# Optimization experiments

Measured on AMD Instinct MI355X. Metric: run time of the kernel, lower is better.

## Reference

```python
import jax, jax.numpy as jnp
import numpy as np

EMBED = 512
HEADS = 8
DIM_HEAD = 64          # embed_dim // 8
LANDMARKS = 256        # embed_dim // 2
PINV_ITERS = 6
RES_K = 33             # nystrom residual_conv_kernel default
SCALE = DIM_HEAD ** -0.5


def layer_norm(x, g, b, eps=1e-5):
    mu = x.mean(-1, keepdims=True)
    var = ((x - mu) ** 2).mean(-1, keepdims=True)
    return (x - mu) / jnp.sqrt(var + eps) * g + b


def moore_penrose_pinv(x, iters=PINV_ITERS):
    # iterative Moore-Penrose pseudo-inverse (lucidrains nystrom-attention)
    ax = jnp.abs(x)
    z = jnp.swapaxes(x, -1, -2) / (ax.sum(-1).max() * ax.sum(-2).max())
    I = jnp.eye(x.shape[-1], dtype=x.dtype)
    for _ in range(iters):
        xz = x @ z
        z = 0.25 * z @ (13. * I - xz @ (15. * I - xz @ (7. * I - xz)))
    return z


def nystrom_attention(x, w_qkv, w_out, b_out, res_k):
    b, n, _ = x.shape
    m = LANDMARKS
    pad = (m - n % m) % m
    xp = jnp.pad(x, ((0, 0), (pad, 0), (0, 0)))  # left-pad like F.pad(..., padding, 0)
    np_ = n + pad
    qkv = (xp @ w_qkv).reshape(b, np_, 3, HEADS, DIM_HEAD)
    q = qkv[:, :, 0].transpose(0, 2, 1, 3) * SCALE   # [b,h,np,dh]
    k = qkv[:, :, 1].transpose(0, 2, 1, 3)
    v = qkv[:, :, 2].transpose(0, 2, 1, 3)
    l = np_ // m
    q_l = q.reshape(b, HEADS, m, l, DIM_HEAD).mean(3)  # [b,h,m,dh]
    k_l = k.reshape(b, HEADS, m, l, DIM_HEAD).mean(3)
    attn1 = jax.nn.softmax(jnp.einsum('bhid,bhjd->bhij', q, k_l), -1)    # [b,h,np,m]
    attn2 = jax.nn.softmax(jnp.einsum('bhid,bhjd->bhij', q_l, k_l), -1)  # [b,h,m,m]
    attn3 = jax.nn.softmax(jnp.einsum('bhid,bhjd->bhij', q_l, k), -1)    # [b,h,m,np]
    out = (attn1 @ moore_penrose_pinv(attn2)) @ (attn3 @ v)              # [b,h,np,dh]
    # depthwise residual conv over the sequence dim, per head (shared across dh)
    v_c = v.transpose(0, 3, 1, 2).reshape(b * DIM_HEAD, HEADS, np_)
    res = jax.lax.conv_general_dilated(
        v_c, res_k[:, None, :], (1,), [(RES_K // 2, RES_K // 2)],
        dimension_numbers=('NCH', 'OIH', 'NCH'), feature_group_count=HEADS)
    out = out + res.reshape(b, DIM_HEAD, HEADS, np_).transpose(0, 2, 3, 1)
    out = out.transpose(0, 2, 1, 3).reshape(b, np_, HEADS * DIM_HEAD)
    out = out @ w_out + b_out
    return out[:, -n:]  # drop left padding


def dwconv2d(x, w, b, k):
    # x: [B,C,H,W], w: [C,1,k,k] depthwise
    y = jax.lax.conv_general_dilated(
        x, w, (1, 1), [(k // 2, k // 2)] * 2,
        dimension_numbers=('NCHW', 'OIHW', 'NCHW'), feature_group_count=x.shape[1])
    return y + b[None, :, None, None]


def ppeg(x, H, W, w7, b7, w5, b5, w3, b3):
    B, _, C = x.shape
    cls_tok, feat = x[:, :1], x[:, 1:]
    f = feat.transpose(0, 2, 1).reshape(B, C, H, W)
    y = f + dwconv2d(f, w7, b7, 7) + dwconv2d(f, w5, b5, 5) + dwconv2d(f, w3, b3, 3)
    y = y.reshape(B, C, H * W).transpose(0, 2, 1)
    return jnp.concatenate([cls_tok, y], axis=1)


def reference(h, w_fc1, b_fc1, cls_token,
              ln1_g, ln1_b, qkv1_w, out1_w, out1_b, res1_k,
              conv7_w, conv7_b, conv5_w, conv5_b, conv3_w, conv3_b,
              ln2_g, ln2_b, qkv2_w, out2_w, out2_b, res2_k,
              lnf_g, lnf_b):
    h = jax.nn.relu(h @ w_fc1 + b_fc1)                 # [B,N,512]
    B, N, C = h.shape
    _H = int(np.ceil(np.sqrt(N)))
    add = _H * _H - N
    h = jnp.concatenate([h, h[:, :add]], axis=1)       # square padding
    h = jnp.concatenate([jnp.broadcast_to(cls_token, (B, 1, C)), h], axis=1)
    h = h + nystrom_attention(layer_norm(h, ln1_g, ln1_b), qkv1_w, out1_w, out1_b, res1_k)
    h = ppeg(h, _H, _H, conv7_w, conv7_b, conv5_w, conv5_b, conv3_w, conv3_b)
    h = h + nystrom_attention(layer_norm(h, ln2_g, ln2_b), qkv2_w, out2_w, out2_b, res2_k)
    return layer_norm(h, lnf_g, lnf_b)[:, 0]           # [B,512]


def setup_inputs() -> dict:
    key = jax.random.key(0)
    ks = jax.random.split(key, 24)
    B, N, IN_DIM = 2, 4096, 1024
    w = lambda k, shape, s=0.02: jax.random.normal(k, shape, jnp.float32) * s
    z = lambda shape: jnp.zeros(shape, jnp.float32)
    o = lambda shape: jnp.ones(shape, jnp.float32)
    return {
        'h': jax.random.normal(ks[0], (B, N, IN_DIM), jnp.float32),
        'w_fc1': w(ks[1], (IN_DIM, EMBED)), 'b_fc1': z((EMBED,)),
        'cls_token': w(ks[2], (1, 1, EMBED)),
        'ln1_g': o((EMBED,)), 'ln1_b': z((EMBED,)),
        'qkv1_w': w(ks[3], (EMBED, 3 * HEADS * DIM_HEAD)),
        'out1_w': w(ks[4], (HEADS * DIM_HEAD, EMBED)), 'out1_b': z((EMBED,)),
        'res1_k': w(ks[5], (HEADS, RES_K), 0.1),
        'conv7_w': w(ks[6], (EMBED, 1, 7, 7), 0.05), 'conv7_b': z((EMBED,)),
        'conv5_w': w(ks[7], (EMBED, 1, 5, 5), 0.05), 'conv5_b': z((EMBED,)),
        'conv3_w': w(ks[8], (EMBED, 1, 3, 3), 0.05), 'conv3_b': z((EMBED,)),
        'ln2_g': o((EMBED,)), 'ln2_b': z((EMBED,)),
        'qkv2_w': w(ks[9], (EMBED, 3 * HEADS * DIM_HEAD)),
        'out2_w': w(ks[10], (HEADS * DIM_HEAD, EMBED)), 'out2_b': z((EMBED,)),
        'res2_k': w(ks[11], (HEADS, RES_K), 0.1),
        'lnf_g': o((EMBED,)), 'lnf_b': z((EMBED,)),
    }
```

## Files before the change

kernel.cpp:

```cpp
#include <hip/hip_runtime.h>
#include <hip/hip_bf16.h>

#define HEADS 8
#define DH 64
#define EMB 512
#define NP 4352
#define NTOK 4097
#define PADF 255
#define LM 256
#define SCALE 0.125f

typedef __attribute__((ext_vector_type(8))) short bf8;
typedef __attribute__((ext_vector_type(4))) float f4;
typedef __attribute__((ext_vector_type(8))) unsigned short us8;
typedef __attribute__((ext_vector_type(4))) unsigned short us4;
typedef unsigned short u16;

__device__ __forceinline__ u16 f2b(float f){
  union { float f; unsigned u; } x; x.f = f;
  unsigned r = x.u + 0x7fffu + ((x.u>>16)&1u);
  return (u16)(r>>16);
}
__device__ __forceinline__ float b2f(u16 h){
  union { unsigned u; float f; } x; x.u = ((unsigned)h)<<16;
  return x.f;
}

__device__ __forceinline__ void gload_lds(const u16* g, u16* l){
  __builtin_amdgcn_global_load_lds((const __attribute__((address_space(1))) void*)g,
                                   (__attribute__((address_space(3))) void*)l, 16, 0, 0);
}

#define WAITCNT(N) asm volatile("s_waitcnt vmcnt(" #N ")" ::: "memory")
#define SCHED_FENCE() __builtin_amdgcn_sched_barrier(0)
#define BARRIER() __builtin_amdgcn_s_barrier()

template<int MODE>
__global__ __launch_bounds__(256)
void k_g128(const u16* __restrict__ A, const u16* __restrict__ B,
            float* __restrict__ C, u16* __restrict__ C16,
            int K, int lda, int ldb, int ldc,
            long sAb, long sAh, long sBb, long sBh, long sCb, long sCh, int nh,
            float alpha, const float* __restrict__ bias, int relu, int rowoff,
            int nx, int ksplit)
{
  int z = blockIdx.z;
  const u16* Ab = A + (long)(z/nh)*sAb + (long)(z%nh)*sAh;
  const u16* Bb = B + (long)(z/nh)*sBb + (long)(z%nh)*sBh;
  long cb = (long)(z/nh)*sCb + (long)(z%nh)*sCh;
  int bx = blockIdx.x % nx, kc = blockIdx.x / nx;
  int m0 = blockIdx.y*128, n0 = bx*128;
  int klen = K/ksplit, kbeg = kc*klen, nch = klen/32;
  __shared__ u16 As[3][4096];
  __shared__ u16 Bs[3][4096];
  int tid=threadIdx.x, w=tid>>6, lane=tid&63, q=lane>>4, lr=lane&15;
  int wrow=(w>>1)*64, wcol=(w&1)*64;
  int srow = tid>>2, scol = (tid&3)*8;
  const u16* ga  = Ab + (long)(m0+srow)*lda + kbeg + scol;
  const u16* ga2 = Ab + (long)(m0+64+srow)*lda + kbeg + scol;
  const u16* gb  = Bb + (long)(n0+srow)*ldb + kbeg + scol;
  const u16* gb2 = Bb + (long)(n0+64+srow)*ldb + kbeg + scol;
  int lo = srow*32 + scol;
  f4 acc[4][4] = {};
  auto stage = [&](int r, int c){
    gload_lds(ga  + c*32, &As[r][lo]);
    gload_lds(ga2 + c*32, &As[r][2048+lo]);
    gload_lds(gb  + c*32, &Bs[r][lo]);
    gload_lds(gb2 + c*32, &Bs[r][2048+lo]);
// ... 86 lines not shown
      acc[t] = __builtin_amdgcn_mfma_f32_16x16x32_bf16(af, bfr, acc[t], 0,0,0);
    }
  };
  stage(0,0);
  if(nch>1) stage(1,1);
  if(nch>2) stage(2,2);
  int bufc = 0;
  for(int c=0;c<nch;c++){
    int rem = nch-1-c;
    if(rem>=2) WAITCNT(4); else if(rem==1) WAITCNT(2); else WAITCNT(0);
    SCHED_FENCE();
    BARRIER();
    compute(bufc);
    SCHED_FENCE();
    BARRIER();
    SCHED_FENCE();
    if(c+3<nch) stage(bufc, c+3);
    bufc = (bufc+1==3)?0:bufc+1;
  }
  #pragma unroll
  for(int t=0;t<4;t++){
    #pragma unroll
    for(int e=0;e<4;e++){
      int gm = m0 + w*16 + q*4 + e;
      int gn = n0 + t*16 + lr;
      float v = acc[t][e]*alpha;
      if(MODE==0) C[cb + (long)gm*ldc + gn] = v;
      else if(MODE==2) C16[cb + (long)gm*ldc + gn] = f2b(v);
      else if(MODE==3) atomicAdd(&C[cb + (long)gm*ldc + gn], v);
      else if(MODE==5){
        v += bias[gn];
        if(gm>=rowoff) C[cb + (long)(gm-rowoff)*ldc + gn] += v;
      }
    }
  }
}

__global__ __launch_bounds__(256)
void k_pg3(const u16* __restrict__ Ah, const u16* __restrict__ Al,
           const u16* __restrict__ Bh, const u16* __restrict__ Bl,
           u16* __restrict__ Oh, u16* __restrict__ Ol, float na, float nd,
           u16* __restrict__ TOh, u16* __restrict__ TOl, float ta, float td)
{
  long zo = (long)blockIdx.z*65536;
  int m0 = blockIdx.y*32, n0 = blockIdx.x*64;
  __shared__ u16 S[3][6144];
  int tid=threadIdx.x, w=tid>>6, lane=tid&63, q=lane>>4, lr=lane&15;
  int t2 = tid & 127;
  const u16* srcA = (tid<128 ? Ah : Al) + zo + (long)(m0 + (t2>>2))*256 + (t2&3)*8;
  const u16* srcBh = Bh + zo + (long)(n0 + (tid>>2))*256 + (tid&3)*8;
  const u16* srcBl = Bl + zo + (long)(n0 + (tid>>2))*256 + (tid&3)*8;
  f4 acc[2] = {};
  auto stage = [&](int r, int c){
    gload_lds(srcA  + c*32, &S[r][tid*8]);
    gload_lds(srcBh + c*32, &S[r][2048 + tid*8]);
    gload_lds(srcBl + c*32, &S[r][4096 + tid*8]);
  };
  int mrow = (w>>1)*16 + lr;
  auto compute = [&](int r){
    bf8 ah = *(const bf8*)&S[r][mrow*32 + q*8];
    bf8 al = *(const bf8*)&S[r][1024 + mrow*32 + q*8];
    #pragma unroll
    for(int t=0;t<2;t++){
      int nrow = (w&1)*32 + t*16 + lr;
      bf8 bh = *(const bf8*)&S[r][2048 + nrow*32 + q*8];
      bf8 bl = *(const bf8*)&S[r][4096 + nrow*32 + q*8];
      acc[t] = __builtin_amdgcn_mfma_f32_16x16x32_bf16(ah, bh, acc[t], 0,0,0);
      acc[t] = __builtin_amdgcn_mfma_f32_16x16x32_bf16(ah, bl, acc[t], 0,0,0);
      acc[t] = __builtin_amdgcn_mfma_f32_16x16x32_bf16(al, bh, acc[t], 0,0,0);
    }
  };
  stage(0,0);
  stage(1,1);
  stage(2,2);
  int bufc = 0;
  for(int c=0;c<8;c++){
    int rem = 7-c;
    if(rem>=2) WAITCNT(6); else if(rem==1) WAITCNT(3); else WAITCNT(0);
    SCHED_FENCE();
    BARRIER();
// ... 2 lines not shown
    BARRIER();
    SCHED_FENCE();
    if(c+3<8) stage(bufc, c+3);
    bufc = (bufc+1==3)?0:bufc+1;
  }
  #pragma unroll
  for(int t=0;t<2;t++){
    int gn = n0 + (w&1)*32 + t*16 + lr;
    if(Oh){
      #pragma unroll
      for(int r=0;r<4;r++){
        int gm = m0 + (w>>1)*16 + q*4 + r;
        float v = na*acc[t][r] + ((gm==gn)?nd:0.f);
        u16 h = f2b(v);
        long o = zo + (long)gm*256 + gn;
        Oh[o] = h; Ol[o] = f2b(v - b2f(h));
      }
    }
    if(TOh){
      us4 th, tl;
      #pragma unroll
      for(int r=0;r<4;r++){
        int gm = m0 + (w>>1)*16 + q*4 + r;
        float v = ta*acc[t][r] + ((gm==gn)?td:0.f);
        u16 h = f2b(v);
        th[r] = h; tl[r] = f2b(v - b2f(h));
      }
      long o = zo + (long)gn*256 + (m0 + (w>>1)*16 + q*4);
      *(us4*)&TOh[o] = th; *(us4*)&TOl[o] = tl;
    }
  }
}

__global__ __launch_bounds__(256)
void k_pg3b(const u16* __restrict__ Zh, const u16* __restrict__ Zl,
            const u16* __restrict__ Ph, const u16* __restrict__ Pl,
            const u16* __restrict__ Bh, const u16* __restrict__ Bl,
            u16* __restrict__ Ozh, u16* __restrict__ Ozl,
            u16* __restrict__ Oyh, u16* __restrict__ Oyl,
            u16* __restrict__ Tyh, u16* __restrict__ Tyl)
{
  long zo = (long)blockIdx.z*65536;
  int ysel = blockIdx.y>>3;
  int m0 = (blockIdx.y&7)*32, n0 = blockIdx.x*64;
  const u16* Ah = ysel ? Ph : Zh;
  const u16* Al = ysel ? Pl : Zl;
  __shared__ u16 S[3][6144];
  int tid=threadIdx.x, w=tid>>6, lane=tid&63, q=lane>>4, lr=lane&15;
  int t2 = tid & 127;
  const u16* srcA = (tid<128 ? Ah : Al) + zo + (long)(m0 + (t2>>2))*256 + (t2&3)*8;
  const u16* srcBh = Bh + zo + (long)(n0 + (tid>>2))*256 + (tid&3)*8;
  const u16* srcBl = Bl + zo + (long)(n0 + (tid>>2))*256 + (tid&3)*8;
  f4 acc[2] = {};
  auto stage = [&](int r, int c){
    gload_lds(srcA  + c*32, &S[r][tid*8]);
    gload_lds(srcBh + c*32, &S[r][2048 + tid*8]);
    gload_lds(srcBl + c*32, &S[r][4096 + tid*8]);
  };
  int mrow = (w>>1)*16 + lr;
  auto compute = [&](int r){
    bf8 ah = *(const bf8*)&S[r][mrow*32 + q*8];
    bf8 al = *(const bf8*)&S[r][1024 + mrow*32 + q*8];
    #pragma unroll
    for(int t=0;t<2;t++){
      int nrow = (w&1)*32 + t*16 + lr;
      bf8 bh = *(const bf8*)&S[r][2048 + nrow*32 + q*8];
      bf8 bl = *(const bf8*)&S[r][4096 + nrow*32 + q*8];
      acc[t] = __builtin_amdgcn_mfma_f32_16x16x32_bf16(ah, bh, acc[t], 0,0,0);
      acc[t] = __builtin_amdgcn_mfma_f32_16x16x32_bf16(ah, bl, acc[t], 0,0,0);
      acc[t] = __builtin_amdgcn_mfma_f32_16x16x32_bf16(al, bh, acc[t], 0,0,0);
    }
  };
  stage(0,0);
  stage(1,1);
  stage(2,2);
  int bufc = 0;
  for(int c=0;c<8;c++){
    int rem = 7-c;
    if(rem>=2) WAITCNT(6); else if(rem==1) WAITCNT(3); else WAITCNT(0);
    SCHED_FENCE();
    BARRIER();
    compute(bufc);
    SCHED_FENCE();
    BARRIER();
    SCHED_FENCE();
    if(c+3<8) stage(bufc, c+3);
    bufc = (bufc+1==3)?0:bufc+1;
  }
  #pragma unroll
  for(int t=0;t<2;t++){
    int gn = n0 + (w&1)*32 + t*16 + lr;
    if(!ysel){
      #pragma unroll
      for(int r=0;r<4;r++){
        int gm = m0 + (w>>1)*16 + q*4 + r;
        float v = 0.25f*acc[t][r];
        u16 h = f2b(v);
        long o = zo + (long)gm*256 + gn;
        Ozh[o] = h; Ozl[o] = f2b(v - b2f(h));
      }
    } else {
      us4 th, tl;
      #pragma unroll
      for(int r=0;r<4;r++){
        int gm = m0 + (w>>1)*16 + q*4 + r;
        float v = 0.25f*acc[t][r];
        u16 h = f2b(v);
        long o = zo + (long)gm*256 + gn;
        Oyh[o] = h; Oyl[o] = f2b(v - b2f(h));
        float tv = -v + ((gm==gn)?7.f:0.f);
        u16 h2 = f2b(tv);
        th[r] = h2; tl[r] = f2b(tv - b2f(h2));
      }
      long o = zo + (long)gn*256 + (m0 + (w>>1)*16 + q*4);
      *(us4*)&Tyh[o] = th; *(us4*)&Tyl[o] = tl;
    }
  }
}

__global__ __launch_bounds__(256)
void k_att2f(const u16* __restrict__ ql, const u16* __restrict__ kl,
             float* __restrict__ att2, float* __restrict__ colsum)
{
  int z = blockIdx.y;
  int m0 = blockIdx.x*64;
  __shared__ u16 SQ[64*64];
  __shared__ u16 SKL[256*64];
  int tid=threadIdx.x, w=tid>>6, lane=tid&63, q=lane>>4, lr=lane&15;
  {
    const u16* qb = ql + (long)z*16384 + m0*64;
    #pragma unroll
    for(int p=0;p<2;p++){
      int idx = tid + p*256; int row = idx>>3; int js = ((idx&7)^(row&7))<<3;
      gload_lds(qb + row*64 + js, &SQ[idx*8]);
    }
    const u16* kb = kl + (long)z*16384;
    #pragma unroll
    for(int p=0;p<8;p++){
      int idx = tid + p*256; int row = idx>>3; int js = ((idx&7)^(row&7))<<3;
      gload_lds(kb + row*64 + js, &SKL[idx*8]);
    }
  }
  __syncthreads();
  f4 acc[16] = {};
  {
    int ar = w*16+lr;
    bf8 af0 = *(const bf8*)&SQ[ar*64 + ((q^(ar&7))<<3)];
    bf8 af1 = *(const bf8*)&SQ[ar*64 + (((q|4)^(ar&7))<<3)];
    #pragma unroll
// ... 165 lines not shown
    #pragma unroll
    for(int kc=0;kc<17;kc++){ mm[kc]=pm[(z*17+kc)*256 + j]; M=fmaxf(M,mm[kc]); }
    float s = 0.f;
    #pragma unroll
    for(int kc=0;kc<17;kc++){ float e=expf(mm[kc]-M); wk[tid][kc]=e; s+=e*pl[(z*17+kc)*256 + j]; }
    float inv = 1.f/s;
    #pragma unroll
    for(int kc=0;kc<17;kc++) wk[tid][kc]*=inv;
  }
  __syncthreads();
  float acc[8];
  #pragma unroll
  for(int p=0;p<8;p++) acc[p]=0.f;
  for(int kc=0;kc<17;kc++){
    long base = ((long)(z*17+kc)*256 + j0)*64;
    #pragma unroll
    for(int p=0;p<8;p++){
      int idx = tid + p*128;
      acc[p] += wk[idx>>6][kc]*partO[base + idx];
    }
  }
  #pragma unroll
  for(int p=0;p<8;p++){ int idx = tid + p*128; T[idx>>6][idx&63] = f2b(acc[p]); }
  __syncthreads();
  int d = tid>>1, jh = (tid&1)*8;
  us8 vv;
  #pragma unroll
  for(int u=0;u<8;u++) vv[u] = T[jh+u][d];
  *(us8*)&avbT16[(long)(z*64+d)*256 + j0 + jh] = vv;
}

__global__ __launch_bounds__(256)
void k_att1(const u16* __restrict__ qkv16, const u16* __restrict__ kl,
            const u16* __restrict__ zavT, float* __restrict__ Qc)
{
  int z = blockIdx.y, b = z>>3, h = z&7;
  int m0 = blockIdx.x*64;
  __shared__ u16 SQ[64*64];
  __shared__ u16 SKL[256*64];
  __shared__ u16 SZV[64*256];
  int tid=threadIdx.x, w=tid>>6, lane=tid&63, q=lane>>4, lr=lane&15;
  {
    const u16* qb = qkv16 + (long)b*NP*1536 + h*64;
    #pragma unroll
    for(int p=0;p<2;p++){
      int idx = tid + p*256; int row = idx>>3; int js = ((idx&7)^(row&7))<<3;
      gload_lds(qb + (long)(m0+row)*1536 + js, &SQ[idx*8]);
    }
    const u16* kb = kl + (long)z*16384;
    #pragma unroll
    for(int p=0;p<8;p++){
      int idx = tid + p*256; int row = idx>>3; int js = ((idx&7)^(row&7))<<3;
      gload_lds(kb + row*64 + js, &SKL[idx*8]);
    }
    const u16* zb = zavT + (long)z*16384;
    #pragma unroll
    for(int p=0;p<8;p++){
      int idx = tid + p*256; int row = idx>>5; int cs = ((idx&31)^(row&7))<<3;
      gload_lds(zb + row*256 + cs, &SZV[idx*8]);
    }
  }
  __syncthreads();
  f4 acc[16] = {};
  {
    int ar = w*16+lr;
    bf8 af0 = *(const bf8*)&SQ[ar*64 + ((q^(ar&7))<<3)];
    bf8 af1 = *(const bf8*)&SQ[ar*64 + (((q|4)^(ar&7))<<3)];
// ... 19 lines not shown
  #pragma unroll
  for(int t=0;t<16;t++)
    #pragma unroll
    for(int e=0;e<4;e++){ float p = expf(acc[t][e]*SCALE - mx[e]); acc[t][e]=p; sm[e]+=p; }
  #pragma unroll
  for(int s=1;s<16;s<<=1)
    #pragma unroll
    for(int e=0;e<4;e++) sm[e] += __shfl_xor(sm[e], s);
  float inv[4];
  #pragma unroll
  for(int e=0;e<4;e++) inv[e] = 1.f/sm[e];
  __syncthreads();
  u16* PS = SKL;
  #pragma unroll
  for(int t=0;t<16;t++)
    #pragma unroll
    for(int e=0;e<4;e++){
      int prow = w*16 + q*4 + e, pcol = t*16 + lr;
      PS[prow*256 + (((pcol>>3)^(prow&7))<<3) + (pcol&7)] = f2b(acc[t][e]*inv[e]);
    }
  __syncthreads();
  f4 acc2[4] = {};
  int pr = w*16+lr;
  #pragma unroll
  for(int ks=0;ks<8;ks++){
    bf8 af = *(const bf8*)&PS[pr*256 + (((ks*4+q)^(pr&7))<<3)];
    #pragma unroll
    for(int t=0;t<4;t++){
      int rr = t*16+lr;
      bf8 bf_ = *(const bf8*)&SZV[rr*256 + (((ks*4+q)^(rr&7))<<3)];
      acc2[t] = __builtin_amdgcn_mfma_f32_16x16x32_bf16(af, bf_, acc2[t], 0,0,0);
    }
  }
  #pragma unroll
  for(int t=0;t<4;t++)
    #pragma unroll
    for(int r=0;r<4;r++){
      int gm = m0 + w*16 + q*4 + r;
      int gd = t*16 + lr;
      Qc[((long)b*NP + gm)*512 + h*64 + gd] = acc2[t][r];
    }
}

__global__ void k_wT(const float* __restrict__ in, u16* __restrict__ out, int K, int N){
  int n0=blockIdx.x*32, k0=blockIdx.y*32, tid=threadIdx.x;
  __shared__ float T[32][33];
  int lr=tid&31, lc=tid>>5;
  #pragma unroll
  for(int p=0;p<4;p++) T[lc+8*p][lr] = in[(long)(k0+lc+8*p)*N + n0+lr];
  __syncthreads();
  #pragma unroll
  for(int p=0;p<4;p++) out[(long)(n0+lc+8*p)*K + k0+lr] = f2b(T[lr][lc+8*p]);
}

__global__ __launch_bounds__(256)
void k_vT(const u16* __restrict__ qkv16, u16* __restrict__ vT){
  int t0=blockIdx.x*64, h=blockIdx.y, b=blockIdx.z, tid=threadIdx.x;
  __shared__ u16 T[64][72];
  const u16* src = qkv16 + (long)b*NP*1536 + 1024 + h*64;
  for(int s=0;s<2;s++){
    int idx=tid+s*256; int row=idx>>3, c8=(idx&7)*8;
    *(us8*)&T[row][c8] = *(const us8*)&src[(long)(t0+row)*1536 + c8];
  }
  __syncthreads();
  u16* dst = vT + ((long)(b*8+h)*64)*NP;
  int d = tid>>2, j0=(tid&3)*16;
  us8 v0,v1;
  #pragma unroll
  for(int jj=0;jj<8;jj++){ v0[jj]=T[j0+jj][d]; v1[jj]=T[j0+8+jj][d]; }
  *(us8*)&dst[(long)d*NP + t0 + j0]     = v0;
  *(us8*)&dst[(long)d*NP + t0 + j0 + 8] = v1;
}

__global__ void k_cvt16(const float* __restrict__ in, u16* __restrict__ out, long n){
  long i = (long)blockIdx.x*256 + threadIdx.x;
  if(i<n) out[i] = f2b(in[i]);
}

__global__ void k_cls(const float* __restrict__ cls, float* __restrict__ seq){
  int b = blockIdx.x;
  seq[(long)b*NTOK*EMB + threadIdx.x] = cls[threadIdx.x];
}

__global__ void k_ln_pad(const float* __restrict__ seq, u16* __restrict__ xp,
                         const float* __restrict__ g, const float* __restrict__ bb){
  int b = blockIdx.y, i = blockIdx.x, tid = threadIdx.x;
  u16* out = xp + ((long)b*NP + i)*EMB;
  if(i < PADF){ out[tid]=0; out[tid+256]=0; return; }
  const float* x = seq + ((long)b*NTOK + (i-PADF))*EMB;
  float v0 = x[tid], v1 = x[tid+256];
  __shared__ float red[256];
  red[tid]=v0+v1; __syncthreads();
  for(int s=128;s>0;s>>=1){ if(tid<s) red[tid]+=red[tid+s]; __syncthreads(); }
  float mu = red[0]*(1.0f/512.0f); __syncthreads();
  float d0=v0-mu, d1=v1-mu;
  red[tid]=d0*d0+d1*d1; __syncthreads();
  for(int s=128;s>0;s>>=1){ if(tid<s) red[tid]+=red[tid+s]; __syncthreads(); }
  float rstd = rsqrtf(red[0]*(1.0f/512.0f) + 1e-5f);
  out[tid]     = f2b(d0*rstd*g[tid]     + bb[tid]);
  out[tid+256] = f2b(d1*rstd*g[tid+256] + bb[tid+256]);
}

__global__ void k_landmarks(const u16* __restrict__ qkv, u16* __restrict__ q_l, u16* __restrict__ k_l,
                            float* __restrict__ colsum){
  if(blockIdx.y==0 && blockIdx.z==0 && blockIdx.x<16) colsum[blockIdx.x*256 + threadIdx.x] = 0.f;
  int j = blockIdx.x*4 + (threadIdx.x>>6), h = blockIdx.y, b = blockIdx.z, d = threadIdx.x&63;
  const u16* base = qkv + (long)b*NP*1536 + h*64 + d;
  float sq=0.f, sk=0.f;
  for(int l=0;l<17;l++){
    long row = (long)(j*17+l)*1536;
    sq += b2f(base[row]);
    sk += b2f(base[row+512]);
  }
  long o = (((long)b*HEADS + h)*LM + j)*DH + d;
  q_l[o] = f2b(sq * (SCALE/17.0f));
  k_l[o] = f2b(sk * (1.0f/17.0f));
}

__global__ void k_pair_init(const float* __restrict__ att2,
    const float* __restrict__ colsum,
    u16* __restrict__ Xh, u16* __restrict__ Xl,
    u16* __restrict__ Zh, u16* __restrict__ Zl,
    u16* __restrict__ Zth, u16* __restrict__ Ztl)
{
  long zo = (long)blockIdx.z*65536;
  int i0 = blockIdx.y*64, j0 = blockIdx.x*64;
  int tid = threadIdx.x;
  __shared__ float cred[256];
  {
    float cm = 0.f;
    #pragma unroll
    for(int i=0;i<16;i++) cm = fmaxf(cm, colsum[tid + i*256]);
    cred[tid] = cm; __syncthreads();
    for(int s=128;s>0;s>>=1){ if(tid<s) cred[tid]=fmaxf(cred[tid],cred[tid+s]); __syncthreads(); }
  }
  float inv = 1.0f/cred[0];
  __syncthreads();
  __shared__ float T[64][68];
  int li = tid>>2, jc = (tid&3)*16;
  #pragma unroll
  for(int u=0;u<4;u++){
    float4 v = *(const float4*)&att2[zo + (long)(i0+li)*256 + j0 + jc + u*4];
    T[li][jc+u*4]=v.x; T[li][jc+u*4+1]=v.y; T[li][jc+u*4+2]=v.z; T[li][jc+u*4+3]=v.w;
    long o = zo + (long)(i0+li)*256 + j0 + jc + u*4;
    float vv[4] = {v.x,v.y,v.z,v.w};
    us4 xh, xl, zth, ztl;
    #pragma unroll
    for(int c=0;c<4;c++){
      u16 h = f2b(vv[c]); xh[c]=h; xl[c]=f2b(vv[c]-b2f(h));
      float zt = vv[c]*inv;
      u16 h2 = f2b(zt); zth[c]=h2; ztl[c]=f2b(zt-b2f(h2));
    }
    *(us4*)&Xh[o]=xh; *(us4*)&Xl[o]=xl; *(us4*)&Zth[o]=zth; *(us4*)&Ztl[o]=ztl;
  }
  __syncthreads();
  int lj = tid>>2, ic = (tid&3)*16;
  #pragma unroll
  for(int r=0;r<16;r++){
    float x = T[ic+r][lj]*inv;
    u16 h = f2b(x);
    long o = zo + (long)(j0+lj)*256 + i0 + ic + r;
    Zh[o]=h; Zl[o]=f2b(x-b2f(h));
  }
}

__global__ __launch_bounds__(256)
void k_rconv(const u16* __restrict__ qkv16, const float* __restrict__ resk,
             const float* __restrict__ Qin, u16* __restrict__ Qo16){
  int t0 = blockIdx.x*64, h = blockIdx.y, b = blockIdx.z;
  __shared__ float V[96*64];
  const u16* vb = qkv16 + (long)b*NP*1536 + 1024 + h*64;
  int tid = threadIdx.x;
  #pragma unroll
  for(int s=0;s<3;s++){
    int idx = tid + s*256;
    int row = idx>>3, c8 = (idx&7)*8;
    int p = t0 - 16 + row;
    if(p>=0 && p<NP){
      us8 v = *(const us8*)&vb[(long)p*1536 + c8];
      #pragma unroll
      for(int jj=0;jj<8;jj++) V[row*64+c8+jj] = b2f(v[jj]);
    } else {
      #pragma unroll
      for(int jj=0;jj<8;jj++) V[row*64+c8+jj] = 0.f;
    }
  }
  __syncthreads();
  int d = tid&63, lt = (tid>>6)*16;
  float acc[16] = {};
  #pragma unroll
  for(int s=0;s<48;s++){
    float val = V[(lt+s)*64 + d];
    #pragma unroll
    for(int j=0;j<16;j++){
      int tap = s - j;
      if(tap>=0 && tap<33) acc[j] += resk[h*33+tap]*val;
    }
  }
  #pragma unroll
  for(int j=0;j<16;j++){
    long idx = ((long)b*NP + t0 + lt + j)*EMB + h*64 + d;
    Qo16[idx] = f2b(Qin[idx] + acc[j]);
  }
}

__global__ __launch_bounds__(256)
void k_ppeg(const float* __restrict__ seq, float* __restrict__ out,
    const float* __restrict__ w7,const float* __restrict__ b7,
    const float* __restrict__ w5,const float* __restrict__ b5,
    const float* __restrict__ w3,const float* __restrict__ b3){
  int b = blockIdx.z, cg = blockIdx.y;
  int rp = blockIdx.x>>1, xs = blockIdx.x&1;
  int ch0 = cg*64;
  __shared__ float s7[64*49], s5[64*25], s3[64*9], sbias[64];
  int tid = threadIdx.x;
  for(int i=tid;i<64*49;i+=256) s7[i] = w7[ch0*49+i];
  for(int i=tid;i<64*25;i+=256) s5[i] = w5[ch0*25+i];
  for(int i=tid;i<64*9;i+=256)  s3[i] = w3[ch0*9+i];
  if(tid<64) sbias[tid] = b7[ch0+tid]+b5[ch0+tid]+b3[ch0+tid];
  if(cg==0 && blockIdx.x==0){
    out[(long)b*NTOK*EMB + tid]       = seq[(long)b*NTOK*EMB + tid];
    out[(long)b*NTOK*EMB + 256 + tid] = seq[(long)b*NTOK*EMB + 256 + tid];
  }
  __syncthreads();
  int c = tid & 63;
  int y = rp*4 + (tid>>6);
  const float* sbase = seq + (long)b*NTOK*EMB + EMB + (ch0 + c);
  float* obase = out + (long)b*NTOK*EMB + EMB + (ch0 + c);
  const float* W7 = &s7[c*49];
  const float* W5 = &s5[c*25];
  const float* W3 = &s3[c*9];
  float bsum = sbias[c];
  for(int xc=0;xc<4;xc++){
    int xb = xs*32 + xc*8;
    float acc[8];
// ... 21 lines not shown
    #pragma unroll
    for(int j=0;j<8;j++) obase[(long)(y*64+xb+j)*EMB] = acc[j];
  }
}

__global__ void k_final_ln(const float* __restrict__ seq, const float* __restrict__ g,
                           const float* __restrict__ bb, float* __restrict__ out){
  int b = blockIdx.x, tid = threadIdx.x;
  const float* x = seq + (long)b*NTOK*EMB;
  float v0 = x[tid], v1 = x[tid+256];
  __shared__ float red[256];
  red[tid]=v0+v1; __syncthreads();
  for(int s=128;s>0;s>>=1){ if(tid<s) red[tid]+=red[tid+s]; __syncthreads(); }
  float mu = red[0]*(1.0f/512.0f); __syncthreads();
  float d0=v0-mu, d1=v1-mu;
  red[tid]=d0*d0+d1*d1; __syncthreads();
  for(int s=128;s>0;s>>=1){ if(tid<s) red[tid]+=red[tid+s]; __syncthreads(); }
  float rstd = rsqrtf(red[0]*(1.0f/512.0f) + 1e-5f);
  out[b*512+tid]     = d0*rstd*g[tid]     + bb[tid];
  out[b*512+tid+256] = d1*rstd*g[tid+256] + bb[tid+256];
}

extern "C" void kernel_launch(void* const* d_in, const int* in_sizes, int n_in,
                              void* d_out, int out_size, void* d_ws, size_t ws_size,
                              hipStream_t stream) {
  const float* in[24];
  for(int i=0;i<24;i++) in[i] = (const float*)d_in[i];

  float* W = (float*)d_ws;
  size_t off = 0;
  float* seqA = W+off; off += 4195328;
  float* seqB = W+off; off += 4195328;
  float* att2 = W+off; off += 1048576;
  float* Qc   = W+off; off += 4456448;
  float* partO= W+off; off += 17825792;
  float* pm   = W+off; off += 69632;
  float* pl   = W+off; off += 69632;
  u16* xpb    = (u16*)(W+off); off += 2228224;
  u16* qkvb16 = (u16*)(W+off); off += 6684672;
  u16* vT16   = (u16*)(W+off); off += 2228224;
  u16* q_l16  = (u16*)(W+off); off += 131072;
  u16* k_l16  = (u16*)(W+off); off += 131072;
  u16* avbT16 = (u16*)(W+off); off += 131072;
  u16* zavT16 = (u16*)(W+off); off += 131072;
  u16* Qc16   = (u16*)(W+off); off += 2228224;
  u16* qkvwT1 = (u16*)(W+off); off += 393216;
  u16* qkvwT2 = (u16*)(W+off); off += 393216;
  u16* outwT1 = (u16*)(W+off); off += 131072;
  u16* outwT2 = (u16*)(W+off); off += 131072;
  u16* pairs  = (u16*)(W+off); off += 9437184;
  float* colsum = W+off; off += 4096;
  if (ws_size < off*sizeof(float)) return;

  u16* h16   = pairs;
  u16* wfc1T = pairs + 8388608;

  const long PB = 1048576;
  u16 *Xh=pairs,        *Xl=pairs+PB;
  u16 *Z0h=pairs+2*PB,  *Z0l=pairs+3*PB;
  u16 *Z0th=pairs+4*PB, *Z0tl=pairs+5*PB;
  u16 *Z1h=pairs+6*PB,  *Z1l=pairs+7*PB;
  u16 *P0h=pairs+8*PB,  *P0l=pairs+9*PB;
  u16 *P1h=pairs+10*PB, *P1l=pairs+11*PB;
  u16 *Tth=pairs+12*PB, *Ttl=pairs+13*PB;
  u16 *Uth=pairs+14*PB, *Utl=pairs+15*PB;
  u16 *Vth=pairs+16*PB, *Vtl=pairs+17*PB;

  k_cvt16<<<32768,256,0,stream>>>(in[0], h16, 8388608L);
  k_wT<<<dim3(16,32),256,0,stream>>>(in[1],  wfc1T, 1024, 512);
  k_wT<<<dim3(48,16),256,0,stream>>>(in[6],  qkvwT1, 512, 1536);
  k_wT<<<dim3(48,16),256,0,stream>>>(in[18], qkvwT2, 512, 1536);
  k_wT<<<dim3(16,16),256,0,stream>>>(in[7],  outwT1, 512, 512);
  k_wT<<<dim3(16,16),256,0,stream>>>(in[19], outwT2, 512, 512);

  k_g128<0><<<dim3(4,32,2),256,0,stream>>>(h16, wfc1T, seqA+EMB, nullptr,
      1024, 1024,1024,512, 4194304L,0, 0,0, (long)NTOK*EMB,0, 1, 1.0f, in[2], 1, 0, 4, 1);
  k_cls<<<2,512,0,stream>>>(in[3], seqA);

  auto attention = [&](float* seq, const float* lng,const float* lnb,
                       const u16* qkvwT, const u16* outwT, const float* outb, const float* resk){
    k_ln_pad<<<dim3(NP,2),256,0,stream>>>(seq, xpb, lng, lnb);
    k_g128<2><<<dim3(12,34,2),256,0,stream>>>(xpb, qkvwT, nullptr, qkvb16,
        512, 512,512,1536, (long)NP*512,0, 0,0, (long)NP*1536,0, 1, 1.0f, nullptr, 0, 0, 12, 1);
    k_landmarks<<<dim3(64,HEADS,2),256,0,stream>>>(qkvb16, q_l16, k_l16, colsum);
    k_vT<<<dim3(68,8,2),256,0,stream>>>(qkvb16, vT16);
    k_att2f<<<dim3(4,16),256,0,stream>>>(q_l16, k_l16, att2, colsum);
    k_pair_init<<<dim3(4,4,16),256,0,stream>>>(att2, colsum, Xh,Xl, Z0h,Z0l, Z0th,Z0tl);
    dim3 pgrid(4,8,16);
    k_pg3<<<pgrid,256,0,stream>>>(Xh,Xl, Z0th,Z0tl, P0h,P0l,1.0f,0.f, Tth,Ttl,-1.0f,7.f);
    for(int it=0; it<6; it++){
      u16 *Zh_=(it&1)?Z1h:Z0h, *Zl_=(it&1)?Z1l:Z0l;
      u16 *Nh_=(it&1)?Z0h:Z1h, *Nl_=(it&1)?Z0l:Z1l;
      u16 *Pch=(it&1)?P1h:P0h, *Pcl=(it&1)?P1l:P0l;
      u16 *Pnh=(it&1)?P0h:P1h, *Pnl=(it&1)?P0l:P1l;
      k_pg3<<<pgrid,256,0,stream>>>(Pch,Pcl, Tth,Ttl, nullptr,nullptr,0.f,0.f, Uth,Utl,-1.0f,15.f);
      k_pg3<<<pgrid,256,0,stream>>>(Pch,Pcl, Uth,Utl, nullptr,nullptr,0.f,0.f, Vth,Vtl,-1.0f,13.f);
      if(it<5) k_pg3b<<<dim3(4,16,16),256,0,stream>>>(Zh_,Zl_, Pch,Pcl, Vth,Vtl,
                                                      Nh_,Nl_, Pnh,Pnl, Tth,Ttl);
      else     k_pg3<<<pgrid,256,0,stream>>>(Zh_,Zl_, Vth,Vtl, Nh_,Nl_,0.25f,0.f,
                                             nullptr,nullptr,0.f,0.f);
    }
    k_att3<<<dim3(17,4,16),256,0,stream>>>(qkvb16, q_l16, vT16, partO, pm, pl);
    k_mrg3<<<dim3(16,16),128,0,stream>>>(partO, pm, pl, avbT16);
    k_g64<2><<<dim3(4,1,16),256,0,stream>>>(avbT16, Z0h, nullptr, zavT16,
        256, 256,256,256, 0,16384L, 0,65536L, 0,16384L, 16, 1.0f, nullptr, 0, 0, 4, 1);
    k_att1<<<dim3(68,16),256,0,stream>>>(qkvb16, k_l16, zavT16, Qc);
    k_rconv<<<dim3(68,8,2),256,0,stream>>>(qkvb16, resk, Qc, Qc16);
    k_g64<5><<<dim3(8,65,2),256,0,stream>>>(Qc16, outwT, seq, nullptr,
        512, 512,512,512, (long)NP*512,0, 0,0, (long)NTOK*EMB,0, 1, 1.0f, outb, PADF, 192, 8, 1);
  };

  attention(seqA, in[4], in[5], qkvwT1, outwT1, in[8], in[9]);
  k_ppeg<<<dim3(32,8,2),256,0,stream>>>(seqA, seqB, in[10],in[11],in[12],in[13],in[14],in[15]);
  attention(seqB, in[16], in[17], qkvwT2, outwT2, in[20], in[21]);
  k_final_ln<<<2,256,0,stream>>>(seqB, in[22], in[23], (float*)d_out);
}
```

Before: 850.1 us.

## Fuse pinv iteration kernels into one persistent kernel with grid barriers

Replaces the roughly 19 separate k_pg3/k_pg3b launches of the Moore-Penrose iteration with a single persistent kernel of 512 blocks that syncs between GEMM stages using a software atomic grid barrier. The barrier counter is reset inside k_landmarks. The goal is to remove per-launch overhead and the tail idle between the many small dependent GEMMs. The change relies on all 512 blocks being co-resident, with launch bounds requesting 2 blocks per CU, or the kernel deadlocks. The Z and P updates now run as two sequential tiles in the same block rather than as a 2x-wide grid.

```diff
diff --git a/kernel.cpp b/kernel.cpp
--- a/kernel.cpp
+++ b/kernel.cpp
@@ -34,6 +34,22 @@
 #define WAITCNT(N) asm volatile("s_waitcnt vmcnt(" #N ")" ::: "memory")
 #define SCHED_FENCE() __builtin_amdgcn_sched_barrier(0)
 #define BARRIER() __builtin_amdgcn_s_barrier()
+
+__device__ __forceinline__ void gridbar(unsigned* bar, unsigned nblk){
+  __syncthreads();
+  if(threadIdx.x==0){
+    __threadfence();
+    unsigned g = atomicAdd(&bar[1], 0u);
+    if(atomicAdd(&bar[0], 1u) == nblk-1u){
+      atomicExch(&bar[0], 0u);
+      atomicAdd(&bar[1], 1u);
+    } else {
+      while(atomicAdd(&bar[1], 0u) == g) __builtin_amdgcn_s_sleep(1);
+    }
+    __threadfence();
+  }
+  __syncthreads();
+}
 
 template<int MODE>
 __global__ __launch_bounds__(256)
@@ -190,16 +206,13 @@
   }
 }
 
-__global__ __launch_bounds__(256)
-void k_pg3(const u16* __restrict__ Ah, const u16* __restrict__ Al,
-           const u16* __restrict__ Bh, const u16* __restrict__ Bl,
-           u16* __restrict__ Oh, u16* __restrict__ Ol, float na, float nd,
-           u16* __restrict__ TOh, u16* __restrict__ TOl, float ta, float td)
+__device__ __forceinline__ void pg3_tile(int tid, int m0, int n0, long zo,
+    const u16* Ah, const u16* Al, const u16* Bh, const u16* Bl,
+    u16* Oh, u16* Ol, float na, float nd,
+    u16* TOh, u16* TOl, float ta, float td,
+    u16 S[3][6144])
 {
-  long zo = (long)blockIdx.z*65536;
-  int m0 = blockIdx.y*32, n0 = blockIdx.x*64;
-  __shared__ u16 S[3][6144];
-  int tid=threadIdx.x, w=tid>>6, lane=tid&63, q=lane>>4, lr=lane&15;
+  int w=tid>>6, lane=tid&63, q=lane>>4, lr=lane&15;
   int t2 = tid & 127;
   const u16* srcA = (tid<128 ? Ah : Al) + zo + (long)(m0 + (t2>>2))*256 + (t2&3)*8;
   const u16* srcBh = Bh + zo + (long)(n0 + (tid>>2))*256 + (tid&3)*8;
@@ -268,89 +281,35 @@
   }
 }
 
-__global__ __launch_bounds__(256)
-void k_pg3b(const u16* __restrict__ Zh, const u16* __restrict__ Zl,
-            const u16* __restrict__ Ph, const u16* __restrict__ Pl,
-            const u16* __restrict__ Bh, const u16* __restrict__ Bl,
-            u16* __restrict__ Ozh, u16* __restrict__ Ozl,
-            u16* __restrict__ Oyh, u16* __restrict__ Oyl,
-            u16* __restrict__ Tyh, u16* __restrict__ Tyl)
+__global__ __launch_bounds__(256, 2)
+void k_pinv_all(const u16* __restrict__ Xh, const u16* __restrict__ Xl,
+                u16* Z0h, u16* Z0l, const u16* __restrict__ Z0th, const u16* __restrict__ Z0tl,
+                u16* Z1h, u16* Z1l,
+                u16* P0h, u16* P0l, u16* P1h, u16* P1l,
+                u16* Tth, u16* Ttl, u16* Uth, u16* Utl, u16* Vth, u16* Vtl,
+                unsigned* bar)
 {
+  __shared__ u16 S[3][6144];
+  int tid = threadIdx.x;
   long zo = (long)blockIdx.z*65536;
-  int ysel = blockIdx.y>>3;
-  int m0 = (blockIdx.y&7)*32, n0 = blockIdx.x*64;
-  const u16* Ah = ysel ? Ph : Zh;
-  const u16* Al = ysel ? Pl : Zl;
-  __shared__ u16 S[3][6144];
-  int tid=threadIdx.x, w=tid>>6, lane=tid&63, q=lane>>4, lr=lane&15;
-  int t2 = tid & 127;
-  const u16* srcA = (tid<128 ? Ah : Al) + zo + (long)(m0 + (t2>>2))*256 + (t2&3)*8;
-  const u16* srcBh = Bh + zo + (long)(n0 + (tid>>2))*256 + (tid&3)*8;
-  const u16* srcBl = Bl + zo + (long)(n0 + (tid>>2))*256 + (tid&3)*8;
-  f4 acc[2] = {};
-  auto stage = [&](int r, int c){
-    gload_lds(srcA  + c*32, &S[r][tid*8]);
-    gload_lds(srcBh + c*32, &S[r][2048 + tid*8]);
-    gload_lds(srcBl + c*32, &S[r][4096 + tid*8]);
-  };
-  int mrow = (w>>1)*16 + lr;
-  auto compute = [&](int r){
-    bf8 ah = *(const bf8*)&S[r][mrow*32 + q*8];
-    bf8 al = *(const bf8*)&S[r][1024 + mrow*32 + q*8];
-    #pragma unroll
-    for(int t=0;t<2;t++){
-      int nrow = (w&1)*32 + t*16 + lr;
-      bf8 bh = *(const bf8*)&S[r][2048 + nrow*32 + q*8];
-      bf8 bl = *(const bf8*)&S[r][4096 + nrow*32 + q*8];
-      acc[t] = __builtin_amdgcn_mfma_f32_16x16x32_bf16(ah, bh, acc[t], 0,0,0);
-      acc[t] = __builtin_amdgcn_mfma_f32_16x16x32_bf16(ah, bl, acc[t], 0,0,0);
-      acc[t] = __builtin_amdgcn_mfma_f32_16x16x32_bf16(al, bh, acc[t], 0,0,0);
-    }
-  };
-  stage(0,0);
-  stage(1,1);
-  stage(2,2);
-  int bufc = 0;
-  for(int c=0;c<8;c++){
-    int rem = 7-c;
-    if(rem>=2) WAITCNT(6); else if(rem==1) WAITCNT(3); else WAITCNT(0);
-    SCHED_FENCE();
-    BARRIER();
-    compute(bufc);
-    SCHED_FENCE();
-    BARRIER();
-    SCHED_FENCE();
-    if(c+3<8) stage(bufc, c+3);
-    bufc = (bufc+1==3)?0:bufc+1;
-  }
-  #pragma unroll
-  for(int t=0;t<2;t++){
-    int gn = n0 + (w&1)*32 + t*16 + lr;
-    if(!ysel){
-      #pragma unroll
-      for(int r=0;r<4;r++){
-        int gm = m0 + (w>>1)*16 + q*4 + r;
-        float v = 0.25f*acc[t][r];
-        u16 h = f2b(v);
-        long o = zo + (long)gm*256 + gn;
-        Ozh[o] = h; Ozl[o] = f2b(v - b2f(h));
-      }
-    } else {
-      us4 th, tl;
-      #pragma unroll
-      for(int r=0;r<4;r++){
-        int gm = m0 + (w>>1)*16 + q*4 + r;
-        float v = 0.25f*acc[t][r];
-        u16 h = f2b(v);
-        long o = zo + (long)gm*256 + gn;
-        Oyh[o] = h; Oyl[o] = f2b(v - b2f(h));
-        float tv = -v + ((gm==gn)?7.f:0.f);
-        u16 h2 = f2b(tv);
-        th[r] = h2; tl[r] = f2b(tv - b2f(h2));
-      }
-      long o = zo + (long)gn*256 + (m0 + (w>>1)*16 + q*4);
-      *(us4*)&Tyh[o] = th; *(us4*)&Tyl[o] = tl;
-    }
+  int m0 = blockIdx.y*32, n0 = blockIdx.x*64;
+  pg3_tile(tid,m0,n0,zo, Xh,Xl, Z0th,Z0tl, P0h,P0l,1.0f,0.f, Tth,Ttl,-1.0f,7.f, S);
+  gridbar(bar, 512);
+  u16 *Zch=Z0h,*Zcl=Z0l,*Znh=Z1h,*Znl=Z1l;
+  u16 *Pch=P0h,*Pcl=P0l,*Pnh=P1h,*Pnl=P1l;
+  for(int it=0; it<6; it++){
+    pg3_tile(tid,m0,n0,zo, Pch,Pcl, Tth,Ttl, nullptr,nullptr,0.f,0.f, Uth,Utl,-1.0f,15.f, S);
+    gridbar(bar, 512);
+    pg3_tile(tid,m0,n0,zo, Pch,Pcl, Uth,Utl, nullptr,nullptr,0.f,0.f, Vth,Vtl,-1.0f,13.f, S);
+    gridbar(bar, 512);
+    pg3_tile(tid,m0,n0,zo, Zch,Zcl, Vth,Vtl, Znh,Znl,0.25f,0.f, nullptr,nullptr,0.f,0.f, S);
+    if(it<5){
+      pg3_tile(tid,m0,n0,zo, Pch,Pcl, Vth,Vtl, Pnh,Pnl,0.25f,0.f, Tth,Ttl,-0.25f,7.f, S);
+      gridbar(bar, 512);
+    }
+    u16* t;
+    t=Zch; Zch=Znh; Znh=t;  t=Zcl; Zcl=Znl; Znl=t;
+    t=Pch; Pch=Pnh; Pnh=t;  t=Pcl; Pcl=Pnl; Pnl=t;
   }
 }
 
@@ -738,8 +697,9 @@
 }
 
 __global__ void k_landmarks(const u16* __restrict__ qkv, u16* __restrict__ q_l, u16* __restrict__ k_l,
-                            float* __restrict__ colsum){
+                            float* __restrict__ colsum, unsigned* __restrict__ bar){
   if(blockIdx.y==0 && blockIdx.z==0 && blockIdx.x<16) colsum[blockIdx.x*256 + threadIdx.x] = 0.f;
+  if(blockIdx.y==0 && blockIdx.z==0 && blockIdx.x==0 && threadIdx.x<2) bar[threadIdx.x] = 0u;
   int j = blockIdx.x*4 + (threadIdx.x>>6), h = blockIdx.y, b = blockIdx.z, d = threadIdx.x&63;
   const u16* base = qkv + (long)b*NP*1536 + h*64 + d;
   float sq=0.f, sk=0.f;
@@ -942,6 +902,7 @@
   u16* outwT2 = (u16*)(W+off); off += 131072;
   u16* pairs  = (u16*)(W+off); off += 9437184;
   float* colsum = W+off; off += 4096;
+  unsigned* bar = (unsigned*)(W+off); off += 4;
   if (ws_size < off*sizeof(float)) return;
 
   u16* h16   = pairs;
@@ -974,24 +935,12 @@
     k_ln_pad<<<dim3(NP,2),256,0,stream>>>(seq, xpb, lng, lnb);
     k_g128<2><<<dim3(12,34,2),256,0,stream>>>(xpb, qkvwT, nullptr, qkvb16,
         512, 512,512,1536, (long)NP*512,0, 0,0, (long)NP*1536,0, 1, 1.0f, nullptr, 0, 0, 12, 1);
-    k_landmarks<<<dim3(64,HEADS,2),256,0,stream>>>(qkvb16, q_l16, k_l16, colsum);
+    k_landmarks<<<dim3(64,HEADS,2),256,0,stream>>>(qkvb16, q_l16, k_l16, colsum, bar);
     k_vT<<<dim3(68,8,2),256,0,stream>>>(qkvb16, vT16);
     k_att2f<<<dim3(4,16),256,0,stream>>>(q_l16, k_l16, att2, colsum);
     k_pair_init<<<dim3(4,4,16),256,0,stream>>>(att2, colsum, Xh,Xl, Z0h,Z0l, Z0th,Z0tl);
-    dim3 pgrid(4,8,16);
-    k_pg3<<<pgrid,256,0,stream>>>(Xh,Xl, Z0th,Z0tl, P0h,P0l,1.0f,0.f, Tth,Ttl,-1.0f,7.f);
-    for(int it=0; it<6; it++){
-      u16 *Zh_=(it&1)?Z1h:Z0h, *Zl_=(it&1)?Z1l:Z0l;
-      u16 *Nh_=(it&1)?Z0h:Z1h, *Nl_=(it&1)?Z0l:Z1l;
-      u16 *Pch=(it&1)?P1h:P0h, *Pcl=(it&1)?P1l:P0l;
-      u16 *Pnh=(it&1)?P0h:P1h, *Pnl=(it&1)?P0l:P1l;
-      k_pg3<<<pgrid,256,0,stream>>>(Pch,Pcl, Tth,Ttl, nullptr,nullptr,0.f,0.f, Uth,Utl,-1.0f,15.f);
-      k_pg3<<<pgrid,256,0,stream>>>(Pch,Pcl, Uth,Utl, nullptr,nullptr,0.f,0.f, Vth,Vtl,-1.0f,13.f);
-      if(it<5) k_pg3b<<<dim3(4,16,16),256,0,stream>>>(Zh_,Zl_, Pch,Pcl, Vth,Vtl,
-                                                      Nh_,Nl_, Pnh,Pnl, Tth,Ttl);
-      else     k_pg3<<<pgrid,256,0,stream>>>(Zh_,Zl_, Vth,Vtl, Nh_,Nl_,0.25f,0.f,
-                                             nullptr,nullptr,0.f,0.f);
-    }
+    k_pinv_all<<<dim3(4,8,16),256,0,stream>>>(Xh,Xl, Z0h,Z0l, Z0th,Z0tl, Z1h,Z1l,
+        P0h,P0l, P1h,P1l, Tth,Ttl, Uth,Utl, Vth,Vtl, bar);
     k_att3<<<dim3(17,4,16),256,0,stream>>>(qkvb16, q_l16, vT16, partO, pm, pl);
     k_mrg3<<<dim3(16,16),128,0,stream>>>(partO, pm, pl, avbT16);
     k_g64<2><<<dim3(4,1,16),256,0,stream>>>(avbT16, Z0h, nullptr, zavT16,
```

New measurement: 2.822 ms. 3.32x slower.

## Fuse residual conv into att1, merge landmark and vT kernels, retile fc1

Applied to the files above, without the earlier changes.

The depthwise residual conv over the sequence is computed inside k_att1 using reused shared memory, so the fp32 Qc intermediate is no longer written and read back and k_rconv disappears. Landmark pooling and the V transpose now run as one launch with block-index dispatch. The fc1 GEMM moves from the 128-tile kernel to the 64-tile kernel with a new fused bias+ReLU epilogue mode. The changes remove launches and a large fp32 round trip, but add shared-memory reuse and a higher register load to k_att1.

```diff
diff --git a/kernel.cpp b/kernel.cpp
--- a/kernel.cpp
+++ b/kernel.cpp
@@ -186,6 +186,10 @@
         v += bias[gn];
         if(gm>=rowoff) C[cb + (long)(gm-rowoff)*ldc + gn] += v;
       }
+      else if(MODE==6){
+        v = fmaxf(v + bias[gn], 0.f);
+        C[cb + (long)gm*ldc + gn] = v;
+      }
     }
   }
 }
@@ -582,7 +586,8 @@
 
 __global__ __launch_bounds__(256)
 void k_att1(const u16* __restrict__ qkv16, const u16* __restrict__ kl,
-            const u16* __restrict__ zavT, float* __restrict__ Qc)
+            const u16* __restrict__ zavT, const float* __restrict__ resk,
+            u16* __restrict__ Qo16)
 {
   int z = blockIdx.y, b = z>>3, h = z&7;
   int m0 = blockIdx.x*64;
@@ -668,14 +673,48 @@
       acc2[t] = __builtin_amdgcn_mfma_f32_16x16x32_bf16(af, bf_, acc2[t], 0,0,0);
     }
   }
+  __syncthreads();
+  float* PO  = (float*)SZV;
+  float* SVW = (float*)SKL;
   #pragma unroll
   for(int t=0;t<4;t++)
     #pragma unroll
-    for(int r=0;r<4;r++){
-      int gm = m0 + w*16 + q*4 + r;
-      int gd = t*16 + lr;
-      Qc[((long)b*NP + gm)*512 + h*64 + gd] = acc2[t][r];
-    }
+    for(int r=0;r<4;r++)
+      PO[(w*16 + q*4 + r)*68 + t*16 + lr] = acc2[t][r];
+  {
+    const u16* vb = qkv16 + (long)b*NP*1536 + 1024 + h*64;
+    #pragma unroll
+    for(int s=0;s<3;s++){
+      int idx = tid + s*256;
+      int row = idx>>3, c8 = (idx&7)*8;
+      int p = m0 - 16 + row;
+      if(p>=0 && p<NP){
+        us8 v = *(const us8*)&vb[(long)p*1536 + c8];
+        #pragma unroll
+        for(int jj=0;jj<8;jj++) SVW[row*64+c8+jj] = b2f(v[jj]);
+      } else {
+        #pragma unroll
+        for(int jj=0;jj<8;jj++) SVW[row*64+c8+jj] = 0.f;
+      }
+    }
+  }
+  __syncthreads();
+  int d = tid&63, lt = (tid>>6)*16;
+  float acc3[16] = {};
+  #pragma unroll
+  for(int s=0;s<48;s++){
+    float val = SVW[(lt+s)*64 + d];
+    #pragma unroll
+    for(int j=0;j<16;j++){
+      int tap = s - j;
+      if(tap>=0 && tap<33) acc3[j] += resk[h*33+tap]*val;
+    }
+  }
+  #pragma unroll
+  for(int j=0;j<16;j++){
+    long idx = ((long)b*NP + m0 + lt + j)*EMB + h*64 + d;
+    Qo16[idx] = f2b(PO[(lt+j)*68 + d] + acc3[j]);
+  }
 }
 
 __global__ void k_wT(const float* __restrict__ in, u16* __restrict__ out, int K, int N){
@@ -690,22 +729,39 @@
 }
 
 __global__ __launch_bounds__(256)
-void k_vT(const u16* __restrict__ qkv16, u16* __restrict__ vT){
-  int t0=blockIdx.x*64, h=blockIdx.y, b=blockIdx.z, tid=threadIdx.x;
+void k_lmvt(const u16* __restrict__ qkv16, u16* __restrict__ q_l, u16* __restrict__ k_l,
+            u16* __restrict__ vT, float* __restrict__ colsum){
+  int h = blockIdx.y, b = blockIdx.z, tid = threadIdx.x;
   __shared__ u16 T[64][72];
-  const u16* src = qkv16 + (long)b*NP*1536 + 1024 + h*64;
-  for(int s=0;s<2;s++){
-    int idx=tid+s*256; int row=idx>>3, c8=(idx&7)*8;
-    *(us8*)&T[row][c8] = *(const us8*)&src[(long)(t0+row)*1536 + c8];
-  }
-  __syncthreads();
-  u16* dst = vT + ((long)(b*8+h)*64)*NP;
-  int d = tid>>2, j0=(tid&3)*16;
-  us8 v0,v1;
-  #pragma unroll
-  for(int jj=0;jj<8;jj++){ v0[jj]=T[j0+jj][d]; v1[jj]=T[j0+8+jj][d]; }
-  *(us8*)&dst[(long)d*NP + t0 + j0]     = v0;
-  *(us8*)&dst[(long)d*NP + t0 + j0 + 8] = v1;
+  if(blockIdx.x < 64){
+    if(blockIdx.y==0 && blockIdx.z==0 && blockIdx.x<16) colsum[blockIdx.x*256 + tid] = 0.f;
+    int j = blockIdx.x*4 + (tid>>6), d = tid&63;
+    const u16* base = qkv16 + (long)b*NP*1536 + h*64 + d;
+    float sq=0.f, sk=0.f;
+    for(int l=0;l<17;l++){
+      long row = (long)(j*17+l)*1536;
+      sq += b2f(base[row]);
+      sk += b2f(base[row+512]);
+    }
+    long o = (((long)b*HEADS + h)*LM + j)*DH + d;
+    q_l[o] = f2b(sq * (SCALE/17.0f));
+    k_l[o] = f2b(sk * (1.0f/17.0f));
+  } else {
+    int t0 = (blockIdx.x-64)*64;
+    const u16* src = qkv16 + (long)b*NP*1536 + 1024 + h*64;
+    for(int s=0;s<2;s++){
+      int idx=tid+s*256; int row=idx>>3, c8=(idx&7)*8;
+      *(us8*)&T[row][c8] = *(const us8*)&src[(long)(t0+row)*1536 + c8];
+    }
+    __syncthreads();
+    u16* dst = vT + ((long)(b*8+h)*64)*NP;
+    int d = tid>>2, j0=(tid&3)*16;
+    us8 v0,v1;
+    #pragma unroll
+    for(int jj=0;jj<8;jj++){ v0[jj]=T[j0+jj][d]; v1[jj]=T[j0+8+jj][d]; }
+    *(us8*)&dst[(long)d*NP + t0 + j0]     = v0;
+    *(us8*)&dst[(long)d*NP + t0 + j0 + 8] = v1;
+  }
 }
 
 __global__ void k_cvt16(const float* __restrict__ in, u16* __restrict__ out, long n){
@@ -737,22 +793,6 @@
   out[tid+256] = f2b(d1*rstd*g[tid+256] + bb[tid+256]);
 }
 
-__global__ void k_landmarks(const u16* __restrict__ qkv, u16* __restrict__ q_l, u16* __restrict__ k_l,
-                            float* __restrict__ colsum){
-  if(blockIdx.y==0 && blockIdx.z==0 && blockIdx.x<16) colsum[blockIdx.x*256 + threadIdx.x] = 0.f;
-  int j = blockIdx.x*4 + (threadIdx.x>>6), h = blockIdx.y, b = blockIdx.z, d = threadIdx.x&63;
-  const u16* base = qkv + (long)b*NP*1536 + h*64 + d;
-  float sq=0.f, sk=0.f;
-  for(int l=0;l<17;l++){
-    long row = (long)(j*17+l)*1536;
-    sq += b2f(base[row]);
-    sk += b2f(base[row+512]);
-  }
-  long o = (((long)b*HEADS + h)*LM + j)*DH + d;
-  q_l[o] = f2b(sq * (SCALE/17.0f));
-  k_l[o] = f2b(sk * (1.0f/17.0f));
-}
-
 __global__ void k_pair_init(const float* __restrict__ att2,
     const float* __restrict__ colsum,
     u16* __restrict__ Xh, u16* __restrict__ Xl,
@@ -797,46 +837,6 @@
     u16 h = f2b(x);
     long o = zo + (long)(j0+lj)*256 + i0 + ic + r;
     Zh[o]=h; Zl[o]=f2b(x-b2f(h));
-  }
-}
-
-__global__ __launch_bounds__(256)
-void k_rconv(const u16* __restrict__ qkv16, const float* __restrict__ resk,
-             const float* __restrict__ Qin, u16* __restrict__ Qo16){
-  int t0 = blockIdx.x*64, h = blockIdx.y, b = blockIdx.z;
-  __shared__ float V[96*64];
-  const u16* vb = qkv16 + (long)b*NP*1536 + 1024 + h*64;
-  int tid = threadIdx.x;
-  #pragma unroll
-  for(int s=0;s<3;s++){
-    int idx = tid + s*256;
-    int row = idx>>3, c8 = (idx&7)*8;
-    int p = t0 - 16 + row;
-    if(p>=0 && p<NP){
-      us8 v = *(const us8*)&vb[(long)p*1536 + c8];
-      #pragma unroll
-      for(int jj=0;jj<8;jj++) V[row*64+c8+jj] = b2f(v[jj]);
-    } else {
-      #pragma unroll
-      for(int jj=0;jj<8;jj++) V[row*64+c8+jj] = 0.f;
-    }
-  }
-  __syncthreads();
-  int d = tid&63, lt = (tid>>6)*16;
-  float acc[16] = {};
-  #pragma unroll
-  for(int s=0;s<48;s++){
-    float val = V[(lt+s)*64 + d];
-    #pragma unroll
-    for(int j=0;j<16;j++){
-      int tap = s - j;
-      if(tap>=0 && tap<33) acc[j] += resk[h*33+tap]*val;
-    }
-  }
-  #pragma unroll
-  for(int j=0;j<16;j++){
-    long idx = ((long)b*NP + t0 + lt + j)*EMB + h*64 + d;
-    Qo16[idx] = f2b(Qin[idx] + acc[j]);
   }
 }
 
@@ -924,7 +924,6 @@
   float* seqA = W+off; off += 4195328;
   float* seqB = W+off; off += 4195328;
   float* att2 = W+off; off += 1048576;
-  float* Qc   = W+off; off += 4456448;
   float* partO= W+off; off += 17825792;
   float* pm   = W+off; off += 69632;
   float* pl   = W+off; off += 69632;
@@ -965,8 +964,8 @@
   k_wT<<<dim3(16,16),256,0,stream>>>(in[7],  outwT1, 512, 512);
   k_wT<<<dim3(16,16),256,0,stream>>>(in[19], outwT2, 512, 512);
 
-  k_g128<0><<<dim3(4,32,2),256,0,stream>>>(h16, wfc1T, seqA+EMB, nullptr,
-      1024, 1024,1024,512, 4194304L,0, 0,0, (long)NTOK*EMB,0, 1, 1.0f, in[2], 1, 0, 4, 1);
+  k_g64<6><<<dim3(8,64,2),256,0,stream>>>(h16, wfc1T, seqA+EMB, nullptr,
+      1024, 1024,1024,512, 4194304L,0, 0,0, (long)NTOK*EMB,0, 1, 1.0f, in[2], 0, 0, 8, 1);
   k_cls<<<2,512,0,stream>>>(in[3], seqA);
 
   auto attention = [&](float* seq, const float* lng,const float* lnb,
@@ -974,8 +973,7 @@
     k_ln_pad<<<dim3(NP,2),256,0,stream>>>(seq, xpb, lng, lnb);
     k_g128<2><<<dim3(12,34,2),256,0,stream>>>(xpb, qkvwT, nullptr, qkvb16,
         512, 512,512,1536, (long)NP*512,0, 0,0, (long)NP*1536,0, 1, 1.0f, nullptr, 0, 0, 12, 1);
-    k_landmarks<<<dim3(64,HEADS,2),256,0,stream>>>(qkvb16, q_l16, k_l16, colsum);
-    k_vT<<<dim3(68,8,2),256,0,stream>>>(qkvb16, vT16);
+    k_lmvt<<<dim3(132,HEADS,2),256,0,stream>>>(qkvb16, q_l16, k_l16, vT16, colsum);
     k_att2f<<<dim3(4,16),256,0,stream>>>(q_l16, k_l16, att2, colsum);
     k_pair_init<<<dim3(4,4,16),256,0,stream>>>(att2, colsum, Xh,Xl, Z0h,Z0l, Z0th,Z0tl);
     dim3 pgrid(4,8,16);
@@ -996,8 +994,7 @@
     k_mrg3<<<dim3(16,16),128,0,stream>>>(partO, pm, pl, avbT16);
     k_g64<2><<<dim3(4,1,16),256,0,stream>>>(avbT16, Z0h, nullptr, zavT16,
         256, 256,256,256, 0,16384L, 0,65536L, 0,16384L, 16, 1.0f, nullptr, 0, 0, 4, 1);
-    k_att1<<<dim3(68,16),256,0,stream>>>(qkvb16, k_l16, zavT16, Qc);
-    k_rconv<<<dim3(68,8,2),256,0,stream>>>(qkvb16, resk, Qc, Qc16);
+    k_att1<<<dim3(68,16),256,0,stream>>>(qkvb16, k_l16, zavT16, resk, Qc16);
     k_g64<5><<<dim3(8,65,2),256,0,stream>>>(Qc16, outwT, seq, nullptr,
         512, 512,512,512, (long)NP*512,0, 0,0, (long)NTOK*EMB,0, 1, 1.0f, outb, PADF, 192, 8, 1);
   };
```

New measurement: 831.4 us (median of 2 runs). 2.2% less time.
